# Kernel tuning notes

Hardware: AMD Instinct MI355X
Metric: run time of the kernel (lower is better)

The kernel has to match this reference:

```python
import jax, jax.numpy as jnp
import numpy as np

HIDDEN = 1024
STATE = 16
DT_RANK = 64


def setup_inputs() -> dict:
    key = jax.random.key(0)
    ks = jax.random.split(key, 5)
    B, S = 2, 2048
    x = jax.random.normal(ks[0], (B, S, HIDDEN), dtype=jnp.float32)
    # lecun_normal-ish init scales
    W_xproj = jax.random.normal(ks[1], (HIDDEN, STATE * 2 + DT_RANK), dtype=jnp.float32) / np.sqrt(HIDDEN)
    W_dt = jax.random.normal(ks[2], (DT_RANK, HIDDEN), dtype=jnp.float32) / np.sqrt(DT_RANK)
    b_dt = jnp.zeros((HIDDEN,), dtype=jnp.float32)
    A_log = jax.random.normal(ks[3], (STATE, HIDDEN), dtype=jnp.float32) / np.sqrt(STATE)
    return {"x": x, "W_xproj": W_xproj, "W_dt": W_dt, "b_dt": b_dt, "A_log": A_log}


def reference(x, W_xproj, W_dt, b_dt, A_log):
    # x: [B, S, D]
    xp = x @ W_xproj                       # [B, S, 2N + R]
    Bm = xp[..., :STATE]                    # [B, S, N]
    Cm = xp[..., STATE:2 * STATE]           # [B, S, N]
    dt = jax.nn.softplus(xp[..., 2 * STATE:] @ W_dt + b_dt)  # [B, S, D]
    A = -jnp.exp(A_log)                     # [N, D]
    A_bar = jnp.exp(A[None, None] * dt[:, :, None, :])        # [B, S, N, D]
    Bu = Bm[:, :, :, None] * dt[:, :, None, :] * x[:, :, None, :]  # [B, S, N, D]

    def scan_fn(h, inp):
        A_t, Bu_t = inp
        h = A_t * h + Bu_t
        return h, h

    h0 = jnp.zeros(Bu.shape[:1] + Bu.shape[2:], dtype=x.dtype)   # [B, N, D]
    _, h_all = jax.lax.scan(scan_fn, h0,
                            (A_bar.transpose(1, 0, 2, 3), Bu.transpose(1, 0, 2, 3)))  # [S, B, N, D]
    y = jnp.einsum('bsn,sbnd->bsd', Cm, h_all)  # [B, S, D]
    return y
```

## Files before the change

kernel.cpp:

```cpp
#include <hip/hip_runtime.h>
#include <math.h>

#define HIDDEN 1024
#define NSTATE 16
#define DTRANK 64
#define BB 2
#define SS 2048
#define ROWS (BB*SS)
#define XPC 96
#define CH 64
#define CL 32
#define BND (BB*NSTATE*HIDDEN)
#define LOG2E 1.44269504088896f

#define RT 64
#define KSPL 8
#define RX (ROWS*XPC)

__global__ __launch_bounds__(256) void k_xproj2(const float* __restrict__ x,
                                                const float* __restrict__ W,
                                                float* __restrict__ part) {
    __shared__ float xs[RT * 32];
    __shared__ float wt[96 * 36];
    int t  = threadIdx.x;
    int rt = blockIdx.x >> 3;
    int ks = blockIdx.x & 7;
    int r0 = rt * RT;
    int k0 = ks * 128;
    int cg = t & 15, rg = t >> 4;

    float acc[4][6];
    #pragma unroll
    for (int a = 0; a < 4; ++a)
        #pragma unroll
        for (int b = 0; b < 6; ++b) acc[a][b] = 0.f;

    for (int ch = 0; ch < 4; ++ch) {
        int kc = k0 + ch * 32;
        __syncthreads();
        #pragma unroll
        for (int m = 0; m < 2; ++m) {
            int e = t + m * 256;
            int row = e >> 3, kb = e & 7;
            float4 v = *(const float4*)&x[(r0 + row) * HIDDEN + kc + kb * 4];
            int kbp = kb ^ ((row >> 2) & 7);
            *(float4*)&xs[row * 32 + kbp * 4] = v;
        }
        #pragma unroll
        for (int m = 0; m < 3; ++m) {
            int f = t + m * 256;
            int kr = f / 24, cq = f % 24;
            float4 v = *(const float4*)&W[(kc + kr) * XPC + cq * 4];
            wt[(cq * 4 + 0) * 36 + kr] = v.x;
            wt[(cq * 4 + 1) * 36 + kr] = v.y;
            wt[(cq * 4 + 2) * 36 + kr] = v.z;
            wt[(cq * 4 + 3) * 36 + kr] = v.w;
        }
        __syncthreads();
        #pragma unroll
        for (int kg = 0; kg < 8; ++kg) {
            float4 wv[6], xv[4];
            #pragma unroll
            for (int j = 0; j < 6; ++j)
                wv[j] = *(float4*)&wt[(cg + 16 * j) * 36 + kg * 4];
            #pragma unroll
            for (int rr = 0; rr < 4; ++rr) {
                int row = rg * 4 + rr;
                xv[rr] = *(float4*)&xs[row * 32 + ((kg ^ ((row >> 2) & 7)) * 4)];
            }
            #pragma unroll
            for (int rr = 0; rr < 4; ++rr)
                #pragma unroll
                for (int j = 0; j < 6; ++j) {
                    acc[rr][j] = fmaf(xv[rr].x, wv[j].x, acc[rr][j]);
                    acc[rr][j] = fmaf(xv[rr].y, wv[j].y, acc[rr][j]);
                    acc[rr][j] = fmaf(xv[rr].z, wv[j].z, acc[rr][j]);
                    acc[rr][j] = fmaf(xv[rr].w, wv[j].w, acc[rr][j]);
                }
        }
    }
    #pragma unroll
    for (int rr = 0; rr < 4; ++rr)
        #pragma unroll
        for (int j = 0; j < 6; ++j)
            part[ks * RX + (r0 + rg * 4 + rr) * XPC + cg + 16 * j] = acc[rr][j];
}

__global__ __launch_bounds__(256)
void k_fused2(const float* __restrict__ part, const float* __restrict__ Wdt,
              const float* __restrict__ bdt, const float* __restrict__ x,
              const float* __restrict__ Alog, float* __restrict__ xp,
              float* __restrict__ dt, float* __restrict__ P,
              float* __restrict__ Q) {
    __shared__ float lx[CL * XPC];
    int t = threadIdx.x;
    int bid = blockIdx.x;
    int dblk = bid & 3;
    int b = (bid >> 2) & 1;
    int c = bid >> 3;
    int row0 = b * SS + c * CL;
    int d = dblk * 256 + t;

    #pragma unroll
    for (int m = 0; m < CL * XPC / 256; ++m) {
        int e = t + m * 256;
        int rl = e / XPC, col = e % XPC;
        int gi = (row0 + rl) * XPC + col;
        float s = 0.f;
        #pragma unroll
        for (int p = 0; p < KSPL; ++p) s += part[p * RX + gi];
        lx[e] = s;
        if (dblk == 0) xp[gi] = s;
    }
    __syncthreads();

    float dtv[CL];
    {
        float bv = bdt[d];
        #pragma unroll
        for (int rr = 0; rr < CL; ++rr) dtv[rr] = bv;
        #pragma unroll 4
        for (int k = 0; k < DTRANK; ++k) {
            float w = Wdt[k * HIDDEN + d];
            #pragma unroll
            for (int rr = 0; rr < CL; ++rr)
                dtv[rr] = fmaf(lx[rr * XPC + 2 * NSTATE + k], w, dtv[rr]);
        }
        #pragma unroll
        for (int rr = 0; rr < CL; ++rr) {
            float a = dtv[rr];
            float o = fmaxf(a, 0.f) + __logf(1.f + __expf(-fabsf(a)));
            dtv[rr] = o;
            dt[(row0 + rr) * HIDDEN + d] = o;
        }
    }

    float A2[NSTATE], Pv[NSTATE], Qv[NSTATE];
    #pragma unroll
    for (int n = 0; n < NSTATE; ++n) {
        A2[n] = -__expf(Alog[n*HIDDEN + d]) * LOG2E;
        Pv[n] = 1.f; Qv[n] = 0.f;
    }
    #pragma unroll 2
    for (int i = 0; i < CL; ++i) {
        float dv = dtv[i];
        float xv = x[(row0 + i) * HIDDEN + d];
        float bx = dv * xv;
        #pragma unroll
        for (int n = 0; n < NSTATE; ++n) {
            float a = exp2f(A2[n] * dv);
            Qv[n] = fmaf(a, Qv[n], lx[i * XPC + n] * bx);
            Pv[n] *= a;
        }
    }
    int base = b * (NSTATE * HIDDEN) + d;
    #pragma unroll
    for (int n = 0; n < NSTATE; ++n) {
        P[c*BND + base + n*HIDDEN] = Pv[n];
        Q[c*BND + base + n*HIDDEN] = Qv[n];
    }
}

__global__ void k_pass2(float* __restrict__ P, const float* __restrict__ Q) {
    int bnd = blockIdx.x * 256 + threadIdx.x;
    float h = 0.f;
    for (int cb = 0; cb < CH / 16; ++cb) {
        float p[16], q[16];
        #pragma unroll
        for (int j = 0; j < 16; ++j) {
            int idx = (cb*16 + j)*BND + bnd;
            p[j] = P[idx]; q[j] = Q[idx];
        }
        #pragma unroll
        for (int j = 0; j < 16; ++j) {
            int idx = (cb*16 + j)*BND + bnd;
            P[idx] = h;
            h = fmaf(p[j], h, q[j]);
        }
    }
}

__global__ __launch_bounds__(256, 4)
void k_pass3(const float* __restrict__ x, const float* __restrict__ dt,
             const float* __restrict__ xp, const float* __restrict__ Alog,
             const float* __restrict__ Hs, float* __restrict__ y) {
    int bid = blockIdx.x;
    int dblk = bid & 3;
    int b = (bid >> 2) & 1;
    int c = bid >> 3;
    int d = dblk * 256 + threadIdx.x;

    float A2[NSTATE], h[NSTATE];
    #pragma unroll
    for (int n = 0; n < NSTATE; ++n) {
        A2[n] = -__expf(Alog[n*HIDDEN + d]) * LOG2E;
        h[n] = Hs[c*BND + b*(NSTATE*HIDDEN) + n*HIDDEN + d];
    }
    int s0 = c * CL;
    #pragma unroll 2
    for (int i = 0; i < CL; ++i) {
        int r = b*SS + s0 + i;
        float dv = dt[r*HIDDEN + d];
        float xv = x[r*HIDDEN + d];
        float bx = dv * xv;
        float bm[NSTATE], cm[NSTATE];
        *(float4*)&bm[0]  = *(const float4*)&xp[r*XPC + 0];
        *(float4*)&bm[4]  = *(const float4*)&xp[r*XPC + 4];
        *(float4*)&bm[8]  = *(const float4*)&xp[r*XPC + 8];
        *(float4*)&bm[12] = *(const float4*)&xp[r*XPC + 12];
        *(float4*)&cm[0]  = *(const float4*)&xp[r*XPC + 16];
        *(float4*)&cm[4]  = *(const float4*)&xp[r*XPC + 20];
        *(float4*)&cm[8]  = *(const float4*)&xp[r*XPC + 24];
        *(float4*)&cm[12] = *(const float4*)&xp[r*XPC + 28];
        float yv = 0.f;
        #pragma unroll
        for (int n = 0; n < NSTATE; ++n) {
            float a = exp2f(A2[n] * dv);
            h[n] = fmaf(a, h[n], bm[n] * bx);
            yv = fmaf(cm[n], h[n], yv);
        }
        y[r*HIDDEN + d] = yv;
    }
}

extern "C" void kernel_launch(void* const* d_in, const int* in_sizes, int n_in,
                              void* d_out, int out_size, void* d_ws, size_t ws_size,
                              hipStream_t stream) {
    const float* x    = (const float*)d_in[0];
    const float* Wx   = (const float*)d_in[1];
    const float* Wdt  = (const float*)d_in[2];
    const float* bdt  = (const float*)d_in[3];
    const float* Alog = (const float*)d_in[4];
    float* y  = (float*)d_out;
    float* ws = (float*)d_ws;

    float* xp   = ws;
    float* dt   = xp + RX;
    float* part = dt + ROWS*HIDDEN;
    float* P    = part + (size_t)KSPL*RX;
    float* Q    = P + (size_t)CH*BND;

    k_xproj2<<<(ROWS/RT)*KSPL, 256, 0, stream>>>(x, Wx, part);
    k_fused2<<<CH*BB*4, 256, 0, stream>>>(part, Wdt, bdt, x, Alog, xp, dt, P, Q);
    k_pass2<<<BND/256, 256, 0, stream>>>(P, Q);
    k_pass3<<<CH*BB*4, 256, 0, stream>>>(x, dt, xp, Alog, P, y);
}
```

Before: 105.6 us.

## Split split-K reduction into separate kernel and read xp directly in fused scan

Moves the reduction of the eight split-K partial sums out of k_fused2 into a new vectorized k_reduce kernel, so each row block no longer redoes the reduction once per hidden block. k_fused2 now keeps Wdt in registers and reads xp rows straight from global memory (uniform addresses that can become scalar loads) instead of staging them in shared memory, and its chunk loop is fully unrolled. k_pass3 also reads B/C coefficients directly instead of copying them into local arrays. The change adds one kernel launch, and the 64 Wdt registers per thread raise register pressure.

```diff
diff --git a/kernel.cpp b/kernel.cpp
--- a/kernel.cpp
+++ b/kernel.cpp
@@ -86,13 +86,23 @@
             part[ks * RX + (r0 + rg * 4 + rr) * XPC + cg + 16 * j] = acc[rr][j];
 }
 
+__global__ void k_reduce(const float* __restrict__ part, float* __restrict__ xp) {
+    int i = (blockIdx.x * 256 + threadIdx.x) * 4;
+    float4 s = *(const float4*)&part[i];
+    #pragma unroll
+    for (int p = 1; p < KSPL; ++p) {
+        float4 v = *(const float4*)&part[p * RX + i];
+        s.x += v.x; s.y += v.y; s.z += v.z; s.w += v.w;
+    }
+    *(float4*)&xp[i] = s;
+}
+
 __global__ __launch_bounds__(256)
-void k_fused2(const float* __restrict__ part, const float* __restrict__ Wdt,
+void k_fused2(const float* __restrict__ xp, const float* __restrict__ Wdt,
               const float* __restrict__ bdt, const float* __restrict__ x,
-              const float* __restrict__ Alog, float* __restrict__ xp,
+              const float* __restrict__ Alog,
               float* __restrict__ dt, float* __restrict__ P,
               float* __restrict__ Q) {
-    __shared__ float lx[CL * XPC];
     int t = threadIdx.x;
     int bid = blockIdx.x;
     int dblk = bid & 3;
@@ -101,38 +111,21 @@
     int row0 = b * SS + c * CL;
     int d = dblk * 256 + t;
 
-    #pragma unroll
-    for (int m = 0; m < CL * XPC / 256; ++m) {
-        int e = t + m * 256;
-        int rl = e / XPC, col = e % XPC;
-        int gi = (row0 + rl) * XPC + col;
-        float s = 0.f;
-        #pragma unroll
-        for (int p = 0; p < KSPL; ++p) s += part[p * RX + gi];
-        lx[e] = s;
-        if (dblk == 0) xp[gi] = s;
-    }
-    __syncthreads();
-
+    float w[DTRANK];
+    #pragma unroll
+    for (int k = 0; k < DTRANK; ++k) w[k] = Wdt[k * HIDDEN + d];
+    float bv = bdt[d];
     float dtv[CL];
-    {
-        float bv = bdt[d];
-        #pragma unroll
-        for (int rr = 0; rr < CL; ++rr) dtv[rr] = bv;
-        #pragma unroll 4
-        for (int k = 0; k < DTRANK; ++k) {
-            float w = Wdt[k * HIDDEN + d];
-            #pragma unroll
-            for (int rr = 0; rr < CL; ++rr)
-                dtv[rr] = fmaf(lx[rr * XPC + 2 * NSTATE + k], w, dtv[rr]);
-        }
-        #pragma unroll
-        for (int rr = 0; rr < CL; ++rr) {
-            float a = dtv[rr];
-            float o = fmaxf(a, 0.f) + __logf(1.f + __expf(-fabsf(a)));
-            dtv[rr] = o;
-            dt[(row0 + rr) * HIDDEN + d] = o;
-        }
+    #pragma unroll
+    for (int rr = 0; rr < CL; ++rr) {
+        const float* xr = xp + (row0 + rr) * XPC + 2 * NSTATE;
+        float acc = bv;
+        #pragma unroll
+        for (int k = 0; k < DTRANK; ++k)
+            acc = fmaf(xr[k], w[k], acc);
+        float o = fmaxf(acc, 0.f) + __logf(1.f + __expf(-fabsf(acc)));
+        dtv[rr] = o;
+        dt[(row0 + rr) * HIDDEN + d] = o;
     }
 
     float A2[NSTATE], Pv[NSTATE], Qv[NSTATE];
@@ -141,15 +134,16 @@
         A2[n] = -__expf(Alog[n*HIDDEN + d]) * LOG2E;
         Pv[n] = 1.f; Qv[n] = 0.f;
     }
-    #pragma unroll 2
+    #pragma unroll
     for (int i = 0; i < CL; ++i) {
+        const float* xr = xp + (row0 + i) * XPC;
         float dv = dtv[i];
         float xv = x[(row0 + i) * HIDDEN + d];
         float bx = dv * xv;
         #pragma unroll
         for (int n = 0; n < NSTATE; ++n) {
             float a = exp2f(A2[n] * dv);
-            Qv[n] = fmaf(a, Qv[n], lx[i * XPC + n] * bx);
+            Qv[n] = fmaf(a, Qv[n], xr[n] * bx);
             Pv[n] *= a;
         }
     }
@@ -200,24 +194,16 @@
     #pragma unroll 2
     for (int i = 0; i < CL; ++i) {
         int r = b*SS + s0 + i;
+        const float* xr = xp + r * XPC;
         float dv = dt[r*HIDDEN + d];
         float xv = x[r*HIDDEN + d];
         float bx = dv * xv;
-        float bm[NSTATE], cm[NSTATE];
-        *(float4*)&bm[0]  = *(const float4*)&xp[r*XPC + 0];
-        *(float4*)&bm[4]  = *(const float4*)&xp[r*XPC + 4];
-        *(float4*)&bm[8]  = *(const float4*)&xp[r*XPC + 8];
-        *(float4*)&bm[12] = *(const float4*)&xp[r*XPC + 12];
-        *(float4*)&cm[0]  = *(const float4*)&xp[r*XPC + 16];
-        *(float4*)&cm[4]  = *(const float4*)&xp[r*XPC + 20];
-        *(float4*)&cm[8]  = *(const float4*)&xp[r*XPC + 24];
-        *(float4*)&cm[12] = *(const float4*)&xp[r*XPC + 28];
         float yv = 0.f;
         #pragma unroll
         for (int n = 0; n < NSTATE; ++n) {
             float a = exp2f(A2[n] * dv);
-            h[n] = fmaf(a, h[n], bm[n] * bx);
-            yv = fmaf(cm[n], h[n], yv);
+            h[n] = fmaf(a, h[n], xr[n] * bx);
+            yv = fmaf(xr[NSTATE + n], h[n], yv);
         }
         y[r*HIDDEN + d] = yv;
     }
@@ -241,7 +227,8 @@
     float* Q    = P + (size_t)CH*BND;
 
     k_xproj2<<<(ROWS/RT)*KSPL, 256, 0, stream>>>(x, Wx, part);
-    k_fused2<<<CH*BB*4, 256, 0, stream>>>(part, Wdt, bdt, x, Alog, xp, dt, P, Q);
+    k_reduce<<<RX/4/256, 256, 0, stream>>>(part, xp);
+    k_fused2<<<CH*BB*4, 256, 0, stream>>>(xp, Wdt, bdt, x, Alog, dt, P, Q);
     k_pass2<<<BND/256, 256, 0, stream>>>(P, Q);
     k_pass3<<<CH*BB*4, 256, 0, stream>>>(x, dt, xp, Alog, P, y);
 }
```

After: 127.1 us. 1.2x slower.
